# Performance work log

Hardware: AMD Instinct MI355X
Metric: run time of the kernel (lower is better)

The kernel has to match this reference:

```python
import jax, jax.numpy as jnp
import numpy as np

N = 100000       # nodes
E = 1600000      # edges per graph
D_IN, D_H, D_OUT = 256, 64, 32
TEM = (0.9, 0.8)  # tem[0], tem[1]


def setup_inputs() -> dict:
    key = jax.random.key(0)
    ks = jax.random.split(key, 17)
    f32 = jnp.float32
    return {
        "features": jax.random.normal(ks[0], (N, D_IN), f32),
        # GraphConv layer1: glorot-ish weight [in, out] + bias
        "W1": jax.random.normal(ks[1], (D_IN, D_H), f32) / np.sqrt(D_IN).astype(np.float32),
        "b1": jnp.zeros((D_H,), f32),
        "W2": jax.random.normal(ks[2], (D_H, D_OUT), f32) / np.sqrt(D_H).astype(np.float32),
        "b2": jnp.zeros((D_OUT,), f32),
        # gating linears: nn.Linear(2*d, 1) -> weight [1, 2*d], bias [1]
        "ga11_w": jax.random.normal(ks[3], (1, 2 * D_H), f32) * 0.1,
        "ga11_b": jnp.zeros((1,), f32),
        "ga12_w": jax.random.normal(ks[4], (1, 2 * D_H), f32) * 0.1,
        "ga12_b": jnp.zeros((1,), f32),
        "ga21_w": jax.random.normal(ks[5], (1, 2 * D_OUT), f32) * 0.1,
        "ga21_b": jnp.zeros((1,), f32),
        "ga22_w": jax.random.normal(ks[6], (1, 2 * D_OUT), f32) * 0.1,
        "ga22_b": jnp.zeros((1,), f32),
        # two graphs as edge lists over the same N nodes
        "src1": jax.random.randint(ks[7], (E,), 0, N, jnp.int32),
        "dst1": jax.random.randint(ks[8], (E,), 0, N, jnp.int32),
        "src2": jax.random.randint(ks[9], (E,), 0, N, jnp.int32),
        "dst2": jax.random.randint(ks[10], (E,), 0, N, jnp.int32),
    }


def _graph_conv(feat, W, b, src, dst):
    """DGL GraphConv, norm='both': D_dst^{-1/2} A^T D_src^{-1/2} X W + b.
    in_feats > out_feats for both layers, so W is applied before aggregation."""
    ones = jnp.ones(src.shape[0], feat.dtype)
    deg_out = jnp.clip(jax.ops.segment_sum(ones, src, num_segments=N), 1.0)  # [N]
    deg_in = jnp.clip(jax.ops.segment_sum(ones, dst, num_segments=N), 1.0)   # [N]
    h = (feat * jax.lax.rsqrt(deg_out)[:, None]) @ W                          # [N, d_out]
    agg = jax.ops.segment_sum(h[src], dst, num_segments=N)                    # SpMM scatter-add
    return agg * jax.lax.rsqrt(deg_in)[:, None] + b


def _gate(xa, xb, w, b, tem):
    """Faithful to: ga = softmax(Linear(cat[xa,xb]), dim=1); diag(ga) -> ga[0,0];
    xb' = tem * diag * xb. softmax over a size-1 axis gives ones; dropout is a
    no-op in eval mode."""
    ga = jnp.concatenate([xa, xb], axis=1) @ w.T + b  # [N, 1]
    ga = jax.nn.softmax(ga, axis=1)                   # all ones ([N,1], axis of size 1)
    d = ga[0, 0]                                      # torch.diag of [N,1] -> scalar ga[0,0]
    return tem * d * xb


def reference(features, W1, b1, W2, b2, ga11_w, ga11_b, ga12_w, ga12_b,
              ga21_w, ga21_b, ga22_w, ga22_b, src1, dst1, src2, dst2):
    x11 = _graph_conv(features, W1, b1, src1, dst1)
    x12 = _graph_conv(features, W1, b1, src2, dst2)
    x12 = _gate(x11, x12, ga11_w, ga11_b, TEM[1])
    x11 = _gate(x12, x11, ga12_w, ga12_b, TEM[0])
    x1 = x11 + x12
    x21 = _graph_conv(x1, W2, b2, src1, dst1)
    x22 = _graph_conv(x1, W2, b2, src2, dst2)
    x22 = _gate(x21, x22, ga21_w, ga21_b, TEM[1])
    x21 = _gate(x22, x21, ga22_w, ga22_b, TEM[0])
    return x21 + x22
```

## Files before the change

### kernel.cpp

```cpp
#include <hip/hip_runtime.h>
#include <hip/hip_bf16.h>

#define TEM0 0.9f
#define TEM1 0.8f
#define NPB 256
#define CAP 4608
#define CHUNKE 2048
#define MAXBUCK 512

typedef __attribute__((ext_vector_type(8))) short bf16x8;
typedef __attribute__((ext_vector_type(4))) float f32x4;

static __device__ __forceinline__ short f2bf(float x) {
  union { __hip_bfloat16 h; short s; } u;
  u.h = __float2bfloat16(x);
  return u.s;
}
static __device__ __forceinline__ float bf2f(short s) {
  union { float f; unsigned u; } v;
  v.u = ((unsigned)(unsigned short)s) << 16;
  return v.f;
}

__global__ __launch_bounds__(256) void bucket_gemm(
    const int* __restrict__ src1, const int* __restrict__ dst1,
    const int* __restrict__ src2, const int* __restrict__ dst2,
    int* gcur_d, int* gcur_s,
    int* __restrict__ rawD1, int* __restrict__ rawD2,
    unsigned char* __restrict__ rawS1, unsigned char* __restrict__ rawS2,
    int E, int NCH, int NBUCK,
    const float* __restrict__ X, const short* __restrict__ Wb,
    short* __restrict__ Yb, int n)
{
  __shared__ int outR[CHUNKE];
  __shared__ unsigned char outS[CHUNKE];
  __shared__ unsigned short tickD[CHUNKE];
  __shared__ unsigned short tickS[CHUNKE];
  __shared__ short bktD[CHUNKE];
  __shared__ short bktS[CHUNKE];
  __shared__ int histD[MAXBUCK], histS[MAXBUCK];
  __shared__ int strtD[MAXBUCK], strtS[MAXBUCK];
  __shared__ int baszD[MAXBUCK], baszS[MAXBUCK];
  __shared__ int wsumD[4], wsumS[4];

  const int nbB = 2 * NCH;
  const int nbG = (n + 63) / 64;
  const int half = nbB < nbG ? nbB : nbG;
  int bi = (int)blockIdx.x;
  bool isB;
  int bid;
  if (bi < 2 * half) { isB = ((bi & 1) == 0); bid = bi >> 1; }
  else               { isB = (nbB > nbG);     bid = bi - half; }

  if (isB) {
    int g = 0, cb = bid;
    if (cb >= NCH) { g = 1; cb -= NCH; }
    const int* src = g ? src2 : src1;
    const int* dst = g ? dst2 : dst1;
    int* rawD = g ? rawD2 : rawD1;
    unsigned char* rawS = g ? rawS2 : rawS1;
    int* curD = gcur_d + g * NBUCK;
    int* curS = gcur_s + g * NBUCK;
    int tid = threadIdx.x;
    int lane = tid & 63, wave = tid >> 6;
    int e0 = cb * CHUNKE;
    int K = min(CHUNKE, E - e0);

    histD[tid] = 0; histD[tid + 256] = 0;
    histS[tid] = 0; histS[tid + 256] = 0;
    __syncthreads();

    for (int i = tid; i < K; i += 256) {
      int d = dst[e0 + i], s = src[e0 + i];
      tickD[i] = (unsigned short)atomicAdd(&histD[d >> 8], 1);
      tickS[i] = (unsigned short)atomicAdd(&histS[s >> 8], 1);
    }
    __syncthreads();

    {
      int d0 = histD[2 * tid], d1 = histD[2 * tid + 1];
      int s0 = histS[2 * tid], s1 = histS[2 * tid + 1];
      int dv = d0 + d1, sv = s0 + s1;
      int vd = dv, vs = sv;
#pragma unroll
      for (int off = 1; off < 64; off <<= 1) {
        int td = __shfl_up(vd, off);
        int ts = __shfl_up(vs, off);
        if (lane >= off) { vd += td; vs += ts; }
      }
      if (lane == 63) { wsumD[wave] = vd; wsumS[wave] = vs; }
      __syncthreads();
      int wpD = 0, wpS = 0;
#pragma unroll
      for (int w0 = 0; w0 < 4; ++w0) {
        wpD += (w0 < wave) ? wsumD[w0] : 0;
        wpS += (w0 < wave) ? wsumS[w0] : 0;
      }
      int exD = wpD + vd - dv;
      int exS = wpS + vs - sv;
      strtD[2 * tid] = exD; strtD[2 * tid + 1] = exD + d0;
      strtS[2 * tid] = exS; strtS[2 * tid + 1] = exS + s0;
      for (int b = tid; b < NBUCK; b += 256) {
        int c = histD[b];
        baszD[b] = c ? atomicAdd(&curD[b], c) : 0;
        c = histS[b];
        baszS[b] = c ? atomicAdd(&curS[b], c) : 0;
      }
    }
    __syncthreads();

    for (int i = tid; i < K; i += 256) {
      int d = dst[e0 + i], s = src[e0 + i];
      int bD = d >> 8, bS = s >> 8;
      int qD = strtD[bD] + (int)tickD[i];
      int qS = strtS[bS] + (int)tickS[i];
      outR[qD] = ((d & 255) << 17) | s;
      bktD[qD] = (short)bD;
      outS[qS] = (unsigned char)(s & 255);
      bktS[qS] = (short)bS;
    }
    __syncthreads();

    for (int i = tid; i < K; i += 256) {
      int b = bktD[i];
      int off = baszD[b] + (i - strtD[b]);
      if (off < CAP) rawD[(size_t)b * CAP + off] = outR[i];
    }
    for (int i = tid; i < K; i += 256) {
      int b = bktS[i];
      int off = baszS[b] + (i - strtS[b]);
      if (off < CAP) rawS[(size_t)b * CAP + off] = outS[i];
    }
  } else {
    int w = threadIdx.x >> 6;
    int l = threadIdx.x & 63;
    int row = bid * 64 + w * 16 + (l & 15);
    int rowc = row < n ? row : n - 1;
    int ko = (l >> 4) << 3;

    f32x4 acc[4] = {};
    const float* xrow = X + (size_t)rowc * 256;

#pragma unroll
    for (int kk = 0; kk < 8; ++kk) {
      const float4* p = reinterpret_cast<const float4*>(xrow + kk * 32 + ko);
      float4 a0 = p[0], a1 = p[1];
      bf16x8 af;
      af[0] = f2bf(a0.x); af[1] = f2bf(a0.y); af[2] = f2bf(a0.z); af[3] = f2bf(a0.w);
      af[4] = f2bf(a1.x); af[5] = f2bf(a1.y); af[6] = f2bf(a1.z); af[7] = f2bf(a1.w);
#pragma unroll
      for (int ct = 0; ct < 4; ++ct) {
        bf16x8 bfrag = *reinterpret_cast<const bf16x8*>(Wb + ((size_t)(ct * 8 + kk) * 64 + l) * 8);
        acc[ct] = __builtin_amdgcn_mfma_f32_16x16x32_bf16(af, bfrag, acc[ct], 0, 0, 0);
      }
    }

    int r0 = bid * 64 + w * 16 + ((l >> 4) << 2);
    int c0 = l & 15;
#pragma unroll
    for (int ct = 0; ct < 4; ++ct) {
#pragma unroll
      for (int i = 0; i < 4; ++i) {
        int r = r0 + i;
        if (r < n) Yb[(size_t)r * 64 + ct * 16 + c0] = f2bf(acc[ct][i]);
      }
    }
  }
}

__global__ __launch_bounds__(256) void hist_src(
    const int* __restrict__ gcur_s,
    const unsigned char* __restrict__ rawS1, const unsigned char* __restrict__ rawS2,
    int* __restrict__ co1, int* __restrict__ co2, int NBUCK, int N)
{
  __shared__ int hist[NPB];
  int g = 0, b = blockIdx.x;
  if (b >= NBUCK) { g = 1; b -= NBUCK; }
  const unsigned char* raw = (g ? rawS2 : rawS1) + (size_t)b * CAP;
  int* co = g ? co2 : co1;
  int K = gcur_s[g * NBUCK + b]; if (K > CAP) K = CAP;
  int tid = threadIdx.x;
  hist[tid] = 0;
  __syncthreads();
  for (int j = tid; j < K; j += 256) atomicAdd(&hist[raw[j]], 1);
  __syncthreads();
  int node = b * NPB + tid;
  if (node < N) co[node] = hist[tid];
}

__global__ __launch_bounds__(256) void sort_dst(
    const int* __restrict__ gcur_d,
    const int* __restrict__ rawD1, const int* __restrict__ rawD2,
    unsigned* __restrict__ edata1, unsigned* __restrict__ edata2,
    const int* __restrict__ co1, const int* __restrict__ co2,
    int* __restrict__ ci1, int* __restrict__ ci2,
    int* __restrict__ ns1, int* __restrict__ ns2, int NBUCK, int N)
{
  __shared__ int hist[NPB], strt[NPB];
  __shared__ short tick[CAP];
  __shared__ int sl[CAP];
  __shared__ int wsum[4];
  int g = 0, b = blockIdx.x;
  if (b >= NBUCK) { g = 1; b -= NBUCK; }
  const int* raw = (g ? rawD2 : rawD1) + (size_t)b * CAP;
  unsigned* edata = g ? edata2 : edata1;
  const int* co = g ? co2 : co1;
  const float tem = g ? TEM1 : TEM0;
  int* ci = g ? ci2 : ci1;
  int* ns = g ? ns2 : ns1;
  int K = gcur_d[g * NBUCK + b]; if (K > CAP) K = CAP;
  int tid = threadIdx.x;
  int lane = tid & 63, wave = tid >> 6;

  hist[tid] = 0;
  __syncthreads();
  for (int j = tid; j < K; j += 256)
    tick[j] = (short)atomicAdd(&hist[raw[j] >> 17], 1);
  __syncthreads();
  int h = hist[tid], v = h;
#pragma unroll
  for (int off = 1; off < 64; off <<= 1) {
    int t = __shfl_up(v, off);
    if (lane >= off) v += t;
  }
  if (lane == 63) wsum[wave] = v;
  __syncthreads();
  int wpre = 0;
#pragma unroll
  for (int w0 = 0; w0 < 4; ++w0) wpre += (w0 < wave) ? wsum[w0] : 0;
  strt[tid] = wpre + v - h;
  __syncthreads();
  for (int j = tid; j < K; j += 256) {
    int r = raw[j];
    sl[strt[r >> 17] + tick[j]] = r & 0x1FFFF;
  }
  __syncthreads();
  size_t gbase = (size_t)b * CAP;
  for (int j = tid; j < K; j += 256) {
    int s = sl[j];
    float c = tem * rsqrtf((float)co[s]);
    unsigned cb = (unsigned)(unsigned short)f2bf(c) & 0x7FFFu;
    edata[gbase + j] = (cb << 17) | (unsigned)s;
  }
  int node = b * NPB + tid;
  if (node < N) { ci[node] = hist[tid]; ns[node] = (int)gbase + strt[tid]; }
}

__global__ __launch_bounds__(256) void prep_w1(
    const float* __restrict__ W, short* __restrict__ Wb)
{
  int t = blockIdx.x * 256 + threadIdx.x;
  if (t >= 2048) return;
  int lane = t & 63;
  int kk = (t >> 6) & 7;
  int ct = t >> 9;
  int col = ct * 16 + (lane & 15);
  int k0 = kk * 32 + ((lane >> 4) << 3);
#pragma unroll
  for (int i = 0; i < 8; ++i)
    Wb[(size_t)t * 8 + i] = f2bf(W[(size_t)(k0 + i) * 64 + col]);
}

template<int DIN, int DOUT, int R>
__global__ __launch_bounds__(256) void gemm_rm_bf(
    const float* __restrict__ X, const float* __restrict__ W,
    short* __restrict__ Yb, int n)
{
  __shared__ float Wl[DIN * DOUT];
  for (int i = threadIdx.x; i < DIN * DOUT; i += 256) Wl[i] = W[i];
  __syncthreads();

  const int col = threadIdx.x % DOUT;
  const int rg  = threadIdx.x / DOUT;
  const int rows_per_block = (256 / DOUT) * R;
  const int row0 = blockIdx.x * rows_per_block + rg * R;

  float acc[R];
#pragma unroll
  for (int r = 0; r < R; ++r) acc[r] = 0.f;

  const float4* X4 = reinterpret_cast<const float4*>(X);

  if (row0 + R <= n) {
    for (int k4 = 0; k4 < DIN / 4; ++k4) {
      float w0 = Wl[(4 * k4 + 0) * DOUT + col];
      float w1 = Wl[(4 * k4 + 1) * DOUT + col];
      float w2 = Wl[(4 * k4 + 2) * DOUT + col];
      float w3 = Wl[(4 * k4 + 3) * DOUT + col];
#pragma unroll
      for (int r = 0; r < R; ++r) {
        float4 x = X4[(size_t)(row0 + r) * (DIN / 4) + k4];
        acc[r] = fmaf(x.x, w0, fmaf(x.y, w1, fmaf(x.z, w2, fmaf(x.w, w3, acc[r]))));
      }
    }
#pragma unroll
    for (int r = 0; r < R; ++r)
      Yb[(size_t)(row0 + r) * DOUT + col] = f2bf(acc[r]);
  } else {
    for (int k4 = 0; k4 < DIN / 4; ++k4) {
      float w0 = Wl[(4 * k4 + 0) * DOUT + col];
      float w1 = Wl[(4 * k4 + 1) * DOUT + col];
      float w2 = Wl[(4 * k4 + 2) * DOUT + col];
      float w3 = Wl[(4 * k4 + 3) * DOUT + col];
#pragma unroll
      for (int r = 0; r < R; ++r) {
        if (row0 + r < n) {
          float4 x = X4[(size_t)(row0 + r) * (DIN / 4) + k4];
          acc[r] = fmaf(x.x, w0, fmaf(x.y, w1, fmaf(x.z, w2, fmaf(x.w, w3, acc[r]))));
        }
      }
    }
    for (int r = 0; r < R; ++r)
      if (row0 + r < n) Yb[(size_t)(row0 + r) * DOUT + col] = f2bf(acc[r]);
  }
}

template<int D>
__global__ __launch_bounds__(256) void gather_nodes_bf(
    const int* __restrict__ ci1, const int* __restrict__ ns1, const unsigned* __restrict__ edata1,
    const int* __restrict__ ci2, const int* __restrict__ ns2, const unsigned* __restrict__ edata2,
    const short* __restrict__ Yb, const float* __restrict__ bias,
    float bscale, float* __restrict__ out, int n)
{
  constexpr int LPR = D / 8;
  constexpr int EPI = 64 / LPR;
  int wid  = (blockIdx.x * 256 + threadIdx.x) >> 6;
  int lane = threadIdx.x & 63;
  int grp = lane / LPR;
  int li  = lane % LPR;
  if (wid >= n) return;

  const bf16x8* Y8 = reinterpret_cast<const bf16x8*>(Yb);
  float a1[8], a2[8];
#pragma unroll
  for (int k = 0; k < 8; ++k) { a1[k] = 0.f; a2[k] = 0.f; }

  int len1 = ci1[wid], st1 = ns1[wid];
  int len2 = ci2[wid], st2 = ns2[wid];
  int lmax = len1 > len2 ? len1 : len2;

  for (int j = grp; j < lmax; j += EPI) {
    bool p1 = j < len1, p2 = j < len2;
    unsigned u1 = p1 ? edata1[st1 + j] : 0u;
    unsigned u2 = p2 ? edata2[st2 + j] : 0u;
    float c1 = __uint_as_float((u1 >> 17) << 16);
    float c2 = __uint_as_float((u2 >> 17) << 16);
    int s1 = (int)(u1 & 0x1FFFFu);
    int s2 = (int)(u2 & 0x1FFFFu);
    bf16x8 v1 = Y8[(size_t)s1 * LPR + li];
    bf16x8 v2 = Y8[(size_t)s2 * LPR + li];
#pragma unroll
    for (int k = 0; k < 8; ++k) {
      a1[k] = fmaf(c1, bf2f(v1[k]), a1[k]);
      a2[k] = fmaf(c2, bf2f(v2[k]), a2[k]);
    }
  }

  float r1 = rsqrtf((float)(len1 < 1 ? 1 : len1));
  float r2 = rsqrtf((float)(len2 < 1 ? 1 : len2));
  float acc[8];
#pragma unroll
  for (int k = 0; k < 8; ++k) acc[k] = fmaf(r1, a1[k], r2 * a2[k]);

#pragma unroll
  for (int m = LPR; m < 64; m <<= 1) {
#pragma unroll
    for (int k = 0; k < 8; ++k) acc[k] += __shfl_xor(acc[k], m);
  }

  if (grp == 0) {
    float4 b0 = reinterpret_cast<const float4*>(bias)[li * 2];
    float4 b1v = reinterpret_cast<const float4*>(bias)[li * 2 + 1];
    float4 o0, o1;
    o0.x = fmaf(bscale, b0.x, acc[0]);
    o0.y = fmaf(bscale, b0.y, acc[1]);
    o0.z = fmaf(bscale, b0.z, acc[2]);
    o0.w = fmaf(bscale, b0.w, acc[3]);
    o1.x = fmaf(bscale, b1v.x, acc[4]);
    o1.y = fmaf(bscale, b1v.y, acc[5]);
    o1.z = fmaf(bscale, b1v.z, acc[6]);
    o1.w = fmaf(bscale, b1v.w, acc[7]);
    float4* op = reinterpret_cast<float4*>(out + (size_t)wid * D + li * 8);
    op[0] = o0;
    op[1] = o1;
  }
}

extern "C" void kernel_launch(void* const* d_in, const int* in_sizes, int n_in,
                              void* d_out, int out_size, void* d_ws, size_t ws_size,
                              hipStream_t stream)
{
  const float* features = (const float*)d_in[0];
  const float* W1 = (const float*)d_in[1];
  const float* b1 = (const float*)d_in[2];
  const float* W2 = (const float*)d_in[3];
  const float* b2 = (const float*)d_in[4];
  const int* src1 = (const int*)d_in[13];
  const int* dst1 = (const int*)d_in[14];
  const int* src2 = (const int*)d_in[15];
  const int* dst2 = (const int*)d_in[16];

  const int N = in_sizes[0] / 256;
  const int E = in_sizes[13];
  const int NBUCK = (N + NPB - 1) / NPB;
  const int NCH = (E + CHUNKE - 1) / CHUNKE;

  char* ws = (char*)d_ws;
  int* gcur_d = (int*)ws;
  int* gcur_s = gcur_d + 2 * NBUCK;
  int* rawD1  = gcur_s + 2 * NBUCK;
  int* rawD2  = rawD1 + (size_t)NBUCK * CAP;
  unsigned char* rawS1 = (unsigned char*)(rawD2 + (size_t)NBUCK * CAP);
  unsigned char* rawS2 = rawS1 + (size_t)NBUCK * CAP;
  unsigned* edata1 = (unsigned*)(rawS2 + (size_t)NBUCK * CAP);
  unsigned* edata2 = edata1 + (size_t)NBUCK * CAP;
  int* ci1 = (int*)(edata2 + (size_t)NBUCK * CAP);
  int* ci2 = ci1 + N;
  int* ns1 = ci2 + N;
  int* ns2 = ns1 + N;
  int* co1 = ns2 + N;
  int* co2 = co1 + N;
  short* Yb  = (short*)(co2 + N);
  short* Y2b = Yb + (size_t)N * 64;
  short* Wb  = Y2b + (size_t)N * 32;
  float* x1  = (float*)(Wb + 16384);
  float* out = (float*)d_out;

  (void)hipMemsetAsync(gcur_d, 0, (size_t)4 * NBUCK * sizeof(int), stream);
  prep_w1<<<8, 256, 0, stream>>>(W1, Wb);

  const int nbGemm = (N + 63) / 64;
  bucket_gemm<<<2 * NCH + nbGemm, 256, 0, stream>>>(
      src1, dst1, src2, dst2, gcur_d, gcur_s,
      rawD1, rawD2, rawS1, rawS2, E, NCH, NBUCK,
      features, Wb, Yb, N);

  hist_src<<<2 * NBUCK, 256, 0, stream>>>(gcur_s, rawS1, rawS2, co1, co2, NBUCK, N);
  sort_dst<<<2 * NBUCK, 256, 0, stream>>>(gcur_d, rawD1, rawD2, edata1, edata2,
                                          co1, co2, ci1, ci2, ns1, ns2, NBUCK, N);

  gather_nodes_bf<64><<<(N + 3) / 4, 256, 0, stream>>>(
      ci1, ns1, edata1, ci2, ns2, edata2, Yb, b1, TEM0 + TEM1, x1, N);

  gemm_rm_bf<64, 32, 8><<<(N + 63) / 64, 256, 0, stream>>>(x1, W2, Y2b, N);
  gather_nodes_bf<32><<<(N + 3) / 4, 256, 0, stream>>>(
      ci1, ns1, edata1, ci2, ns2, edata2, Y2b, b2, TEM0 + TEM1, out, N);
}
```

Measured before the change: 291.2 us.

## Merge hist/sort kernels, bf16 x1 with MFMA layer-2 GEMM, compute norms in gather

Fuses the source histogram and destination sort into one launch, with even and odd blocks doing the two independent jobs. The sort no longer needs the source degrees, so the dependency between them goes away. The per-edge coefficient is no longer packed into edata; the gather computes tem*rsqrt(deg_out[src]) on the fly, which adds an extra random co[] load per edge. The intermediate x1 is stored as bf16, and layer 2 uses an MFMA GEMM with a bf16 W2 prepared alongside W1. This reduces traffic and launch count but adds per-edge gather work.

```diff
diff --git a/kernel.cpp b/kernel.cpp
--- a/kernel.cpp
+++ b/kernel.cpp
@@ -168,31 +168,12 @@
   }
 }
 
-__global__ __launch_bounds__(256) void hist_src(
-    const int* __restrict__ gcur_s,
+__global__ __launch_bounds__(256) void histsort(
+    const int* __restrict__ gcur_s, const int* __restrict__ gcur_d,
     const unsigned char* __restrict__ rawS1, const unsigned char* __restrict__ rawS2,
-    int* __restrict__ co1, int* __restrict__ co2, int NBUCK, int N)
-{
-  __shared__ int hist[NPB];
-  int g = 0, b = blockIdx.x;
-  if (b >= NBUCK) { g = 1; b -= NBUCK; }
-  const unsigned char* raw = (g ? rawS2 : rawS1) + (size_t)b * CAP;
-  int* co = g ? co2 : co1;
-  int K = gcur_s[g * NBUCK + b]; if (K > CAP) K = CAP;
-  int tid = threadIdx.x;
-  hist[tid] = 0;
-  __syncthreads();
-  for (int j = tid; j < K; j += 256) atomicAdd(&hist[raw[j]], 1);
-  __syncthreads();
-  int node = b * NPB + tid;
-  if (node < N) co[node] = hist[tid];
-}
-
-__global__ __launch_bounds__(256) void sort_dst(
-    const int* __restrict__ gcur_d,
     const int* __restrict__ rawD1, const int* __restrict__ rawD2,
-    unsigned* __restrict__ edata1, unsigned* __restrict__ edata2,
-    const int* __restrict__ co1, const int* __restrict__ co2,
+    int* __restrict__ co1, int* __restrict__ co2,
+    int* __restrict__ edata1, int* __restrict__ edata2,
     int* __restrict__ ci1, int* __restrict__ ci2,
     int* __restrict__ ns1, int* __restrict__ ns2, int NBUCK, int N)
 {
@@ -200,127 +181,132 @@
   __shared__ short tick[CAP];
   __shared__ int sl[CAP];
   __shared__ int wsum[4];
-  int g = 0, b = blockIdx.x;
+
+  int bi = (int)blockIdx.x;
+  bool isHist = ((bi & 1) == 0);
+  int bid = bi >> 1;
+  int g = 0, b = bid;
   if (b >= NBUCK) { g = 1; b -= NBUCK; }
-  const int* raw = (g ? rawD2 : rawD1) + (size_t)b * CAP;
-  unsigned* edata = g ? edata2 : edata1;
-  const int* co = g ? co2 : co1;
-  const float tem = g ? TEM1 : TEM0;
-  int* ci = g ? ci2 : ci1;
-  int* ns = g ? ns2 : ns1;
-  int K = gcur_d[g * NBUCK + b]; if (K > CAP) K = CAP;
   int tid = threadIdx.x;
-  int lane = tid & 63, wave = tid >> 6;
-
-  hist[tid] = 0;
-  __syncthreads();
-  for (int j = tid; j < K; j += 256)
-    tick[j] = (short)atomicAdd(&hist[raw[j] >> 17], 1);
-  __syncthreads();
-  int h = hist[tid], v = h;
-#pragma unroll
-  for (int off = 1; off < 64; off <<= 1) {
-    int t = __shfl_up(v, off);
-    if (lane >= off) v += t;
-  }
-  if (lane == 63) wsum[wave] = v;
-  __syncthreads();
-  int wpre = 0;
-#pragma unroll
-  for (int w0 = 0; w0 < 4; ++w0) wpre += (w0 < wave) ? wsum[w0] : 0;
-  strt[tid] = wpre + v - h;
-  __syncthreads();
-  for (int j = tid; j < K; j += 256) {
-    int r = raw[j];
-    sl[strt[r >> 17] + tick[j]] = r & 0x1FFFF;
-  }
-  __syncthreads();
-  size_t gbase = (size_t)b * CAP;
-  for (int j = tid; j < K; j += 256) {
-    int s = sl[j];
-    float c = tem * rsqrtf((float)co[s]);
-    unsigned cb = (unsigned)(unsigned short)f2bf(c) & 0x7FFFu;
-    edata[gbase + j] = (cb << 17) | (unsigned)s;
-  }
-  int node = b * NPB + tid;
-  if (node < N) { ci[node] = hist[tid]; ns[node] = (int)gbase + strt[tid]; }
-}
-
-__global__ __launch_bounds__(256) void prep_w1(
-    const float* __restrict__ W, short* __restrict__ Wb)
+
+  if (isHist) {
+    const unsigned char* raw = (g ? rawS2 : rawS1) + (size_t)b * CAP;
+    int* co = g ? co2 : co1;
+    int K = gcur_s[g * NBUCK + b]; if (K > CAP) K = CAP;
+    hist[tid] = 0;
+    __syncthreads();
+    for (int j = tid; j < K; j += 256) atomicAdd(&hist[raw[j]], 1);
+    __syncthreads();
+    int node = b * NPB + tid;
+    if (node < N) co[node] = hist[tid];
+  } else {
+    const int* raw = (g ? rawD2 : rawD1) + (size_t)b * CAP;
+    int* edata = g ? edata2 : edata1;
+    int* ci = g ? ci2 : ci1;
+    int* ns = g ? ns2 : ns1;
+    int K = gcur_d[g * NBUCK + b]; if (K > CAP) K = CAP;
+    int lane = tid & 63, wave = tid >> 6;
+
+    hist[tid] = 0;
+    __syncthreads();
+    for (int j = tid; j < K; j += 256)
+      tick[j] = (short)atomicAdd(&hist[raw[j] >> 17], 1);
+    __syncthreads();
+    int h = hist[tid], v = h;
+#pragma unroll
+    for (int off = 1; off < 64; off <<= 1) {
+      int t = __shfl_up(v, off);
+      if (lane >= off) v += t;
+    }
+    if (lane == 63) wsum[wave] = v;
+    __syncthreads();
+    int wpre = 0;
+#pragma unroll
+    for (int w0 = 0; w0 < 4; ++w0) wpre += (w0 < wave) ? wsum[w0] : 0;
+    strt[tid] = wpre + v - h;
+    __syncthreads();
+    for (int j = tid; j < K; j += 256) {
+      int r = raw[j];
+      sl[strt[r >> 17] + tick[j]] = r & 0x1FFFF;
+    }
+    __syncthreads();
+    size_t gbase = (size_t)b * CAP;
+    for (int j = tid; j < K; j += 256) edata[gbase + j] = sl[j];
+    int node = b * NPB + tid;
+    if (node < N) { ci[node] = hist[tid]; ns[node] = (int)gbase + strt[tid]; }
+  }
+}
+
+__global__ __launch_bounds__(256) void prep_w(
+    const float* __restrict__ W1, const float* __restrict__ W2,
+    short* __restrict__ Wb, short* __restrict__ Wb2)
 {
   int t = blockIdx.x * 256 + threadIdx.x;
-  if (t >= 2048) return;
-  int lane = t & 63;
-  int kk = (t >> 6) & 7;
-  int ct = t >> 9;
-  int col = ct * 16 + (lane & 15);
-  int k0 = kk * 32 + ((lane >> 4) << 3);
-#pragma unroll
-  for (int i = 0; i < 8; ++i)
-    Wb[(size_t)t * 8 + i] = f2bf(W[(size_t)(k0 + i) * 64 + col]);
-}
-
-template<int DIN, int DOUT, int R>
-__global__ __launch_bounds__(256) void gemm_rm_bf(
-    const float* __restrict__ X, const float* __restrict__ W,
-    short* __restrict__ Yb, int n)
-{
-  __shared__ float Wl[DIN * DOUT];
-  for (int i = threadIdx.x; i < DIN * DOUT; i += 256) Wl[i] = W[i];
-  __syncthreads();
-
-  const int col = threadIdx.x % DOUT;
-  const int rg  = threadIdx.x / DOUT;
-  const int rows_per_block = (256 / DOUT) * R;
-  const int row0 = blockIdx.x * rows_per_block + rg * R;
-
-  float acc[R];
-#pragma unroll
-  for (int r = 0; r < R; ++r) acc[r] = 0.f;
-
-  const float4* X4 = reinterpret_cast<const float4*>(X);
-
-  if (row0 + R <= n) {
-    for (int k4 = 0; k4 < DIN / 4; ++k4) {
-      float w0 = Wl[(4 * k4 + 0) * DOUT + col];
-      float w1 = Wl[(4 * k4 + 1) * DOUT + col];
-      float w2 = Wl[(4 * k4 + 2) * DOUT + col];
-      float w3 = Wl[(4 * k4 + 3) * DOUT + col];
-#pragma unroll
-      for (int r = 0; r < R; ++r) {
-        float4 x = X4[(size_t)(row0 + r) * (DIN / 4) + k4];
-        acc[r] = fmaf(x.x, w0, fmaf(x.y, w1, fmaf(x.z, w2, fmaf(x.w, w3, acc[r]))));
-      }
-    }
-#pragma unroll
-    for (int r = 0; r < R; ++r)
-      Yb[(size_t)(row0 + r) * DOUT + col] = f2bf(acc[r]);
-  } else {
-    for (int k4 = 0; k4 < DIN / 4; ++k4) {
-      float w0 = Wl[(4 * k4 + 0) * DOUT + col];
-      float w1 = Wl[(4 * k4 + 1) * DOUT + col];
-      float w2 = Wl[(4 * k4 + 2) * DOUT + col];
-      float w3 = Wl[(4 * k4 + 3) * DOUT + col];
-#pragma unroll
-      for (int r = 0; r < R; ++r) {
-        if (row0 + r < n) {
-          float4 x = X4[(size_t)(row0 + r) * (DIN / 4) + k4];
-          acc[r] = fmaf(x.x, w0, fmaf(x.y, w1, fmaf(x.z, w2, fmaf(x.w, w3, acc[r]))));
-        }
-      }
-    }
-    for (int r = 0; r < R; ++r)
-      if (row0 + r < n) Yb[(size_t)(row0 + r) * DOUT + col] = f2bf(acc[r]);
-  }
-}
-
-template<int D>
+  if (t < 2048) {
+    int lane = t & 63;
+    int kk = (t >> 6) & 7;
+    int ct = t >> 9;
+    int col = ct * 16 + (lane & 15);
+    int k0 = kk * 32 + ((lane >> 4) << 3);
+#pragma unroll
+    for (int i = 0; i < 8; ++i)
+      Wb[(size_t)t * 8 + i] = f2bf(W1[(size_t)(k0 + i) * 64 + col]);
+  } else if (t < 3072) {
+    int t2 = t - 2048;
+    int lane = t2 & 63;
+    int kk = (t2 >> 6) & 1;
+    int ct = t2 >> 7;
+    int col = ct * 16 + (lane & 15);
+    int k0 = kk * 32 + ((lane >> 4) << 3);
+#pragma unroll
+    for (int i = 0; i < 8; ++i)
+      Wb2[(size_t)t2 * 8 + i] = f2bf(W2[(size_t)(k0 + i) * 32 + col]);
+  }
+}
+
+__global__ __launch_bounds__(256) void gemm2_mfma(
+    const short* __restrict__ X, const short* __restrict__ Wb2,
+    short* __restrict__ Y2b, int n)
+{
+  int w = threadIdx.x >> 6;
+  int l = threadIdx.x & 63;
+  int row = blockIdx.x * 64 + w * 16 + (l & 15);
+  int rowc = row < n ? row : n - 1;
+  int ko = (l >> 4) << 3;
+
+  f32x4 acc[2] = {};
+  const short* xrow = X + (size_t)rowc * 64;
+
+#pragma unroll
+  for (int kk = 0; kk < 2; ++kk) {
+    bf16x8 af = *reinterpret_cast<const bf16x8*>(xrow + kk * 32 + ko);
+#pragma unroll
+    for (int ct = 0; ct < 2; ++ct) {
+      bf16x8 bfrag = *reinterpret_cast<const bf16x8*>(Wb2 + ((size_t)(ct * 2 + kk) * 64 + l) * 8);
+      acc[ct] = __builtin_amdgcn_mfma_f32_16x16x32_bf16(af, bfrag, acc[ct], 0, 0, 0);
+    }
+  }
+
+  int r0 = blockIdx.x * 64 + w * 16 + ((l >> 4) << 2);
+  int c0 = l & 15;
+#pragma unroll
+  for (int ct = 0; ct < 2; ++ct) {
+#pragma unroll
+    for (int i = 0; i < 4; ++i) {
+      int r = r0 + i;
+      if (r < n) Y2b[(size_t)r * 32 + ct * 16 + c0] = f2bf(acc[ct][i]);
+    }
+  }
+}
+
+template<int D, bool BF16OUT>
 __global__ __launch_bounds__(256) void gather_nodes_bf(
-    const int* __restrict__ ci1, const int* __restrict__ ns1, const unsigned* __restrict__ edata1,
-    const int* __restrict__ ci2, const int* __restrict__ ns2, const unsigned* __restrict__ edata2,
+    const int* __restrict__ ci1, const int* __restrict__ ns1,
+    const int* __restrict__ edata1, const int* __restrict__ co1,
+    const int* __restrict__ ci2, const int* __restrict__ ns2,
+    const int* __restrict__ edata2, const int* __restrict__ co2,
     const short* __restrict__ Yb, const float* __restrict__ bias,
-    float bscale, float* __restrict__ out, int n)
+    float bscale, float* __restrict__ outf, short* __restrict__ outb, int n)
 {
   constexpr int LPR = D / 8;
   constexpr int EPI = 64 / LPR;
@@ -339,14 +325,13 @@
   int len2 = ci2[wid], st2 = ns2[wid];
   int lmax = len1 > len2 ? len1 : len2;
 
+#pragma unroll 2
   for (int j = grp; j < lmax; j += EPI) {
     bool p1 = j < len1, p2 = j < len2;
-    unsigned u1 = p1 ? edata1[st1 + j] : 0u;
-    unsigned u2 = p2 ? edata2[st2 + j] : 0u;
-    float c1 = __uint_as_float((u1 >> 17) << 16);
-    float c2 = __uint_as_float((u2 >> 17) << 16);
-    int s1 = (int)(u1 & 0x1FFFFu);
-    int s2 = (int)(u2 & 0x1FFFFu);
+    int s1 = p1 ? edata1[st1 + j] : 0;
+    int s2 = p2 ? edata2[st2 + j] : 0;
+    float c1 = p1 ? TEM0 * rsqrtf((float)co1[s1]) : 0.f;
+    float c2 = p2 ? TEM1 * rsqrtf((float)co2[s2]) : 0.f;
     bf16x8 v1 = Y8[(size_t)s1 * LPR + li];
     bf16x8 v2 = Y8[(size_t)s2 * LPR + li];
 #pragma unroll
@@ -371,18 +356,27 @@
   if (grp == 0) {
     float4 b0 = reinterpret_cast<const float4*>(bias)[li * 2];
     float4 b1v = reinterpret_cast<const float4*>(bias)[li * 2 + 1];
-    float4 o0, o1;
-    o0.x = fmaf(bscale, b0.x, acc[0]);
-    o0.y = fmaf(bscale, b0.y, acc[1]);
-    o0.z = fmaf(bscale, b0.z, acc[2]);
-    o0.w = fmaf(bscale, b0.w, acc[3]);
-    o1.x = fmaf(bscale, b1v.x, acc[4]);
-    o1.y = fmaf(bscale, b1v.y, acc[5]);
-    o1.z = fmaf(bscale, b1v.z, acc[6]);
-    o1.w = fmaf(bscale, b1v.w, acc[7]);
-    float4* op = reinterpret_cast<float4*>(out + (size_t)wid * D + li * 8);
-    op[0] = o0;
-    op[1] = o1;
+    float o[8];
+    o[0] = fmaf(bscale, b0.x, acc[0]);
+    o[1] = fmaf(bscale, b0.y, acc[1]);
+    o[2] = fmaf(bscale, b0.z, acc[2]);
+    o[3] = fmaf(bscale, b0.w, acc[3]);
+    o[4] = fmaf(bscale, b1v.x, acc[4]);
+    o[5] = fmaf(bscale, b1v.y, acc[5]);
+    o[6] = fmaf(bscale, b1v.z, acc[6]);
+    o[7] = fmaf(bscale, b1v.w, acc[7]);
+    if constexpr (BF16OUT) {
+      bf16x8 ov;
+#pragma unroll
+      for (int k = 0; k < 8; ++k) ov[k] = f2bf(o[k]);
+      *reinterpret_cast<bf16x8*>(outb + (size_t)wid * D + li * 8) = ov;
+    } else {
+      float4 o0 = make_float4(o[0], o[1], o[2], o[3]);
+      float4 o1 = make_float4(o[4], o[5], o[6], o[7]);
+      float4* op = reinterpret_cast<float4*>(outf + (size_t)wid * D + li * 8);
+      op[0] = o0;
+      op[1] = o1;
+    }
   }
 }
 
@@ -412,9 +406,9 @@
   int* rawD2  = rawD1 + (size_t)NBUCK * CAP;
   unsigned char* rawS1 = (unsigned char*)(rawD2 + (size_t)NBUCK * CAP);
   unsigned char* rawS2 = rawS1 + (size_t)NBUCK * CAP;
-  unsigned* edata1 = (unsigned*)(rawS2 + (size_t)NBUCK * CAP);
-  unsigned* edata2 = edata1 + (size_t)NBUCK * CAP;
-  int* ci1 = (int*)(edata2 + (size_t)NBUCK * CAP);
+  int* edata1 = (int*)(rawS2 + (size_t)NBUCK * CAP);
+  int* edata2 = edata1 + (size_t)NBUCK * CAP;
+  int* ci1 = edata2 + (size_t)NBUCK * CAP;
   int* ci2 = ci1 + N;
   int* ns1 = ci2 + N;
   int* ns2 = ns1 + N;
@@ -422,12 +416,13 @@
   int* co2 = co1 + N;
   short* Yb  = (short*)(co2 + N);
   short* Y2b = Yb + (size_t)N * 64;
-  short* Wb  = Y2b + (size_t)N * 32;
-  float* x1  = (float*)(Wb + 16384);
+  short* x1b = Y2b + (size_t)N * 32;
+  short* Wb  = x1b + (size_t)N * 64;
+  short* Wb2 = Wb + 16384;
   float* out = (float*)d_out;
 
   (void)hipMemsetAsync(gcur_d, 0, (size_t)4 * NBUCK * sizeof(int), stream);
-  prep_w1<<<8, 256, 0, stream>>>(W1, Wb);
+  prep_w<<<12, 256, 0, stream>>>(W1, W2, Wb, Wb2);
 
   const int nbGemm = (N + 63) / 64;
   bucket_gemm<<<2 * NCH + nbGemm, 256, 0, stream>>>(
@@ -435,14 +430,17 @@
       rawD1, rawD2, rawS1, rawS2, E, NCH, NBUCK,
       features, Wb, Yb, N);
 
-  hist_src<<<2 * NBUCK, 256, 0, stream>>>(gcur_s, rawS1, rawS2, co1, co2, NBUCK, N);
-  sort_dst<<<2 * NBUCK, 256, 0, stream>>>(gcur_d, rawD1, rawD2, edata1, edata2,
-                                          co1, co2, ci1, ci2, ns1, ns2, NBUCK, N);
-
-  gather_nodes_bf<64><<<(N + 3) / 4, 256, 0, stream>>>(
-      ci1, ns1, edata1, ci2, ns2, edata2, Yb, b1, TEM0 + TEM1, x1, N);
-
-  gemm_rm_bf<64, 32, 8><<<(N + 63) / 64, 256, 0, stream>>>(x1, W2, Y2b, N);
-  gather_nodes_bf<32><<<(N + 3) / 4, 256, 0, stream>>>(
-      ci1, ns1, edata1, ci2, ns2, edata2, Y2b, b2, TEM0 + TEM1, out, N);
-}
+  histsort<<<4 * NBUCK, 256, 0, stream>>>(
+      gcur_s, gcur_d, rawS1, rawS2, rawD1, rawD2,
+      co1, co2, edata1, edata2, ci1, ci2, ns1, ns2, NBUCK, N);
+
+  gather_nodes_bf<64, true><<<(N + 3) / 4, 256, 0, stream>>>(
+      ci1, ns1, edata1, co1, ci2, ns2, edata2, co2,
+      Yb, b1, TEM0 + TEM1, nullptr, x1b, N);
+
+  gemm2_mfma<<<nbGemm, 256, 0, stream>>>(x1b, Wb2, Y2b, N);
+
+  gather_nodes_bf<32, false><<<(N + 3) / 4, 256, 0, stream>>>(
+      ci1, ns1, edata1, co1, ci2, ns2, edata2, co2,
+      Y2b, b2, TEM0 + TEM1, out, nullptr, N);
+}
```

After: 317.4 us. +9.0%, slower.
